# Optimization experiments

Measured on AMD Instinct MI355X. Metric: run time of the kernel, lower is better.

## Reference

```python
import jax, jax.numpy as jnp
import numpy as np

ALPHA = 0.2  # LeakyReLU negative slope


def setup_inputs() -> dict:
    key = jax.random.key(0)
    k1, k2, k3, k4, k5 = jax.random.split(key, 5)
    N, H, W, T, V, F = 8, 64, 64, 32, 32, 32
    h = jax.random.normal(k1, (N, H, W, T, V), dtype=jnp.float32)
    W_map = jax.random.normal(k2, (T, F), dtype=jnp.float32) * (1.414 / np.sqrt(T))
    b_map = jax.random.normal(k3, (F,), dtype=jnp.float32) * 0.01
    a_attn = jax.random.normal(k4, (2 * F, 1), dtype=jnp.float32) * (1.414 / np.sqrt(2 * F))
    B_adj = jax.random.normal(k5, (V, V), dtype=jnp.float32) * 1e-3 + 1e-6
    return {"h": h, "W_map": W_map, "b_map": b_map, "a_attn": a_attn, "B_adj": B_adj}


def reference(h, W_map, b_map, a_attn, B_adj):
    # h: (N,H,W,T,V) -> (N,V,H,W,T)
    hv = jnp.transpose(h, (0, 4, 1, 2, 3))
    Wh = hv @ W_map + b_map  # (N,V,H,W,F) -- LinearMapping
    N, V, H, W, F = Wh.shape
    # pairwise concat + matmul with a decomposes exactly into two projections
    a1, a2 = a_attn[:F, 0], a_attn[F:, 0]
    e = (jnp.einsum('nihwf,f->nihw', Wh, a1)[:, :, None, :, :]
         + jnp.einsum('njhwf,f->njhw', Wh, a2)[:, None, :, :, :])  # (N,V,V,H,W)
    e = jnp.where(e > 0, e, ALPHA * e)  # LeakyReLU
    attn = jax.nn.softmax(e, axis=-1)  # softmax over the W dim (as in original: dim=-1 of (N,V,V,H,W))
    # normalized adjacency: (B + I), min-max scaled, symmetric degree normalization
    adj = B_adj + jnp.eye(V, dtype=B_adj.dtype)
    adj = (adj - adj.min()) / (adj.max() - adj.min())
    d12 = 1.0 / jnp.sqrt(jnp.sum(adj, axis=1))
    adj_n = d12[:, None] * adj * d12[None, :]  # (V,V)
    # weighted aggregation over source vertices j (the original double for-loop)
    hp = jnp.einsum('nijhw,njhwf->inhwf', attn, Wh)  # (V,N,H,W,F)
    # replicate permute(1,3,4,2,0).view(N,H,W*F,V) @ adj_n
    hp = jnp.transpose(hp, (1, 3, 4, 2, 0)).reshape(N, H, W * F, V)
    hp = (hp @ adj_n).reshape(N, H, W, F, V)
    return jax.nn.elu(hp)
```

## Files before the change

kernel.cpp:

```cpp
#include <hip/hip_runtime.h>
#include <math.h>

typedef __attribute__((ext_vector_type(8))) short bf16x8;
typedef __attribute__((ext_vector_type(16))) float f32x16;
typedef __attribute__((ext_vector_type(4))) float f32x4;

static constexpr size_t WS_WA   = 0;
static constexpr size_t WS_C12  = 64;
static constexpr size_t WS_WMF  = 96;
static constexpr size_t WS_ADJF = 608;

__device__ __forceinline__ unsigned short f2bf(float x){
    union { float f; unsigned u; } c; c.f = x;
    unsigned r = c.u + 0x7FFFu + ((c.u >> 16) & 1u);
    return (unsigned short)(r >> 16);
}
__device__ __forceinline__ unsigned pk2(float a, float b){
    return (unsigned)f2bf(a) | ((unsigned)f2bf(b) << 16);
}
__device__ __forceinline__ float bf2f(unsigned short v){
    return __uint_as_float(((unsigned)v) << 16);
}
__device__ __forceinline__ float elu(float x){ return x > 0.f ? x : __expf(x) - 1.0f; }
__device__ __forceinline__ float lrelu(float x){ return fmaxf(x, 0.2f * x); }

__global__ __launch_bounds__(1024) void k0_prep(const float* __restrict__ W_map,
    const float* __restrict__ b_map, const float* __restrict__ a_attn,
    const float* __restrict__ B_adj, float* __restrict__ ws)
{
    __shared__ float lds[1024];
    __shared__ float d12[32];
    int tid = threadIdx.x;
    int i = tid >> 5, j = tid & 31;
    float a = B_adj[tid] + (i == j ? 1.0f : 0.0f);
    lds[tid] = a; __syncthreads();
    for (int s = 512; s > 0; s >>= 1) { if (tid < s) lds[tid] = fmaxf(lds[tid], lds[tid + s]); __syncthreads(); }
    float mx = lds[0]; __syncthreads();
    lds[tid] = a; __syncthreads();
    for (int s = 512; s > 0; s >>= 1) { if (tid < s) lds[tid] = fminf(lds[tid], lds[tid + s]); __syncthreads(); }
    float mn = lds[0]; __syncthreads();
    lds[tid] = (a - mn) / (mx - mn); __syncthreads();
    if (tid < 32) {
        float s = 0.f;
        for (int jj = 0; jj < 32; ++jj) s += lds[tid * 32 + jj];
        d12[tid] = 1.0f / sqrtf(s);
    }
    __syncthreads();

    {
        int kap = tid >> 9, rem = tid & 511, l = rem >> 3, e = rem & 7;
        int krow = 16 * kap + 8 * (l >> 5) + e;
        int col  = l & 31;
        ((unsigned short*)(ws + WS_WMF))[tid] = f2bf(W_map[krow * 32 + col]);
        float aij = B_adj[krow * 32 + col] + (krow == col ? 1.0f : 0.0f);
        float adjv = d12[krow] * ((aij - mn) / (mx - mn)) * d12[col];
        ((unsigned short*)(ws + WS_ADJF))[tid] = f2bf(adjv);
    }
    if (tid < 32) {
        float w1 = 0.f, w2 = 0.f;
        for (int f = 0; f < 32; ++f) {
            w1 += W_map[tid * 32 + f] * a_attn[f];
            w2 += W_map[tid * 32 + f] * a_attn[32 + f];
        }
        ws[WS_WA + tid] = w1; ws[WS_WA + 32 + tid] = w2;
    }
    if (tid == 0) {
        float c1 = 0.f, c2 = 0.f;
        for (int f = 0; f < 32; ++f) { c1 += b_map[f] * a_attn[f]; c2 += b_map[f] * a_attn[32 + f]; }
        ws[WS_C12] = c1; ws[WS_C12 + 1] = c2;
    }
}

template<int KAP>
__device__ __forceinline__ bf16x8 xform(const f32x16& d, int hi){
    unsigned b0 = pk2(d[8*KAP+0], d[8*KAP+1]);
    unsigned b1 = pk2(d[8*KAP+2], d[8*KAP+3]);
    unsigned b2 = pk2(d[8*KAP+4], d[8*KAP+5]);
    unsigned b3 = pk2(d[8*KAP+6], d[8*KAP+7]);
    unsigned pb0 = (unsigned)__shfl_xor((int)b0, 32, 64);
    unsigned pb1 = (unsigned)__shfl_xor((int)b1, 32, 64);
    unsigned pb2 = (unsigned)__shfl_xor((int)b2, 32, 64);
    unsigned pb3 = (unsigned)__shfl_xor((int)b3, 32, 64);
    union { unsigned u[4]; bf16x8 v; } t;
    t.u[0] = hi ? pb2 : b0;
    t.u[1] = hi ? pb3 : b1;
    t.u[2] = hi ? b2 : pb0;
    t.u[3] = hi ? b3 : pb1;
    return t.v;
}

__global__ __launch_bounds__(1024) void kfused(const float* __restrict__ hin,
    const float* __restrict__ b_map, const float* __restrict__ ws, float* __restrict__ out)
{
    __shared__ unsigned short hbf[64 * 1024];
    __shared__ float s1L[64 * 32];
    __shared__ float s2L[64 * 32];
    __shared__ float rdenL[32 * 32];
    __shared__ float waL[64];

    const int tid = threadIdx.x;
    const int wv = tid >> 6, l = tid & 63;
    const int c = l & 31, hi = l >> 5;
    const int nh = blockIdx.x;
    const int hh = nh & 63, n = nh >> 6;

    if (tid < 64) waL[tid] = ws[WS_WA + tid];
    const float c1 = ws[WS_C12], c2 = ws[WS_C12 + 1];
    const float bc = b_map[c];

    bf16x8 B1f[2], B2f[2];
    {
        const unsigned short* wmf = (const unsigned short*)(ws + WS_WMF);
        const unsigned short* adf = (const unsigned short*)(ws + WS_ADJF);
        B1f[0] = *(const bf16x8*)(wmf + l * 8);
        B1f[1] = *(const bf16x8*)(wmf + 512 + l * 8);
        B2f[0] = *(const bf16x8*)(adf + l * 8);
        B2f[1] = *(const bf16x8*)(adf + 512 + l * 8);
    }

    {
        const float* hrow = hin + (long)nh * 65536;
        unsigned* hb32 = (unsigned*)hbf;
#pragma unroll
        for (int it = 0; it < 8; ++it) {
            int slot = it * 1024 + tid;
            int s = slot >> 7, r = slot & 127;
            int t = (r >> 3) * 2, v0 = (r & 7) * 4;
            f32x4 x0 = *(const f32x4*)(hrow + s * 1024 + t * 32 + v0);
            f32x4 x1 = *(const f32x4*)(hrow + s * 1024 + (t + 1) * 32 + v0);
            int kap = t >> 4, e = t & 7, lb = 32 * ((t >> 3) & 1);
#pragma unroll
            for (int cc = 0; cc < 4; ++cc) {
                int u16i = s * 1024 + kap * 512 + (v0 + cc + lb) * 8 + e;
                hb32[u16i >> 1] = pk2(x0[cc], x1[cc]);
            }
        }
    }
    __syncthreads();

    {
        float wa1v[16], wa2v[16];
#pragma unroll
        for (int kk = 0; kk < 16; ++kk) {
            int t = 16 * (kk >> 3) + 8 * hi + (kk & 7);
            wa1v[kk] = waL[t]; wa2v[kk] = waL[32 + t];
        }
#pragma unroll
        for (int k = 0; k < 4; ++k) {
            int s = wv * 4 + k;
            const unsigned short* fp = hbf + s * 1024;
            bf16x8 f0 = *(const bf16x8*)(fp + l * 8);
            bf16x8 f1 = *(const bf16x8*)(fp + 512 + l * 8);
            float p1 = 0.f, p2 = 0.f;
#pragma unroll
            for (int e = 0; e < 8; ++e) {
                float x = bf2f((unsigned short)f0[e]);
                p1 = fmaf(x, wa1v[e], p1); p2 = fmaf(x, wa2v[e], p2);
            }
#pragma unroll
            for (int e = 0; e < 8; ++e) {
                float x = bf2f((unsigned short)f1[e]);
                p1 = fmaf(x, wa1v[8 + e], p1); p2 = fmaf(x, wa2v[8 + e], p2);
            }
            p1 += __shfl_xor(p1, 32, 64);
            p2 += __shfl_xor(p2, 32, 64);
            if (!hi) { s1L[s * 32 + c] = p1 + c1; s2L[s * 32 + c] = p2 + c2; }
        }
    }
    __syncthreads();

    {
        int i = tid >> 5, j = tid & 31;
        float sum = 0.f;
#pragma unroll
        for (int w = 0; w < 64; ++w)
            sum += __expf(lrelu(s1L[w * 32 + i] + s2L[w * 32 + j]));
        rdenL[tid] = 1.0f / sum;
    }
    __syncthreads();

    const int hh5 = hh >> 5, f3 = hh & 31;
#pragma unroll 1
    for (int k = 0; k < 4; ++k) {
        const int s = wv * 4 + k;
        const unsigned short* fp = hbf + s * 1024;
        bf16x8 a10 = *(const bf16x8*)(fp + l * 8);
        bf16x8 a11 = *(const bf16x8*)(fp + 512 + l * 8);

        f32x16 d1;
#pragma unroll
        for (int r = 0; r < 16; ++r) d1[r] = bc;
        d1 = __builtin_amdgcn_mfma_f32_32x32x16_bf16(a10, B1f[0], d1, 0, 0, 0);
        d1 = __builtin_amdgcn_mfma_f32_32x32x16_bf16(a11, B1f[1], d1, 0, 0, 0);
        bf16x8 A3_0 = xform<0>(d1, hi);
        bf16x8 A3_1 = xform<1>(d1, hi);

        const float s2c = s2L[s * 32 + c];
        f32x4 sa = *(const f32x4*)&s1L[s * 32 + 8 * hi];
        f32x4 sb = *(const f32x4*)&s1L[s * 32 + 8 * hi + 4];
        f32x4 sc_ = *(const f32x4*)&s1L[s * 32 + 16 + 8 * hi];
        f32x4 sd = *(const f32x4*)&s1L[s * 32 + 16 + 8 * hi + 4];
        float q[16];
#pragma unroll
        for (int e = 0; e < 4; ++e) {
            int i0 = 8 * hi + e, i1 = 8 * hi + 4 + e, i2i = 16 + 8 * hi + e, i3 = 16 + 8 * hi + 4 + e;
            q[e]      = __expf(lrelu(sa[e] + s2c)) * rdenL[i0 * 32 + c];
            q[4 + e]  = __expf(lrelu(sb[e] + s2c)) * rdenL[i1 * 32 + c];
            q[8 + e]  = __expf(lrelu(sc_[e] + s2c)) * rdenL[i2i * 32 + c];
            q[12 + e] = __expf(lrelu(sd[e] + s2c)) * rdenL[i3 * 32 + c];
        }
        union { unsigned u[4]; bf16x8 v; } A2_0, A2_1;
        A2_0.u[0] = pk2(q[0], q[1]);  A2_0.u[1] = pk2(q[2], q[3]);
        A2_0.u[2] = pk2(q[4], q[5]);  A2_0.u[3] = pk2(q[6], q[7]);
        A2_1.u[0] = pk2(q[8], q[9]);  A2_1.u[1] = pk2(q[10], q[11]);
        A2_1.u[2] = pk2(q[12], q[13]); A2_1.u[3] = pk2(q[14], q[15]);

        f32x16 d2;
#pragma unroll
        for (int r = 0; r < 16; ++r) d2[r] = 0.f;
        d2 = __builtin_amdgcn_mfma_f32_32x32x16_bf16(A2_0.v, B2f[0], d2, 0, 0, 0);
        d2 = __builtin_amdgcn_mfma_f32_32x32x16_bf16(A2_1.v, B2f[1], d2, 0, 0, 0);
        bf16x8 B3_0 = xform<0>(d2, hi);
        bf16x8 B3_1 = xform<1>(d2, hi);

        f32x16 d3;
#pragma unroll
        for (int r = 0; r < 16; ++r) d3[r] = 0.f;
        d3 = __builtin_amdgcn_mfma_f32_32x32x16_bf16(A3_0, B3_0, d3, 0, 0, 0);
        d3 = __builtin_amdgcn_mfma_f32_32x32x16_bf16(A3_1, B3_1, d3, 0, 0, 0);

        float* ob = out + (((long)(n * 64 + s) * 64) * 32 + f3) * 32 + c;
#pragma unroll
        for (int r = 0; r < 16; ++r) {
            int f = (r & 3) + 8 * (r >> 2) + 4 * hi;
            ob[(f * 2 + hh5) * 1024] = elu(d3[r]);
        }
    }
}

extern "C" void kernel_launch(void* const* d_in, const int* in_sizes, int n_in,
                              void* d_out, int out_size, void* d_ws, size_t ws_size,
                              hipStream_t stream) {
    (void)in_sizes; (void)n_in; (void)out_size; (void)ws_size;
    const float* hin    = (const float*)d_in[0];
    const float* W_map  = (const float*)d_in[1];
    const float* b_map  = (const float*)d_in[2];
    const float* a_attn = (const float*)d_in[3];
    const float* B_adj  = (const float*)d_in[4];
    float* out = (float*)d_out;
    float* ws  = (float*)d_ws;

    hipLaunchKernelGGL(k0_prep, dim3(1),   dim3(1024), 0, stream, W_map, b_map, a_attn, B_adj, ws);
    hipLaunchKernelGGL(kfused,  dim3(512), dim3(1024), 0, stream, hin, b_map, ws, out);
}
```

Measured before the change: 70.68 us.

## Use permlane32_swap, rework bf16 staging loads, nontemporal stores, unroll main loop

Several independent changes. The xform transpose now uses permlane32_swap where the builtin exists, replacing four xor-32 shuffles and selects. The input staging loop loads scalar floats strided by 32 so each thread packs eight bf16 values into one 16-byte LDS store, instead of two float4 loads and four 4-byte stores. Output stores become nontemporal, and the main loop is unrolled by 2 with a launch_bounds minimum-blocks hint of 4. The scalar strided loads may issue more global load instructions, and the unroll may raise register pressure.

```diff
diff --git a/kernel.cpp b/kernel.cpp
--- a/kernel.cpp
+++ b/kernel.cpp
@@ -4,6 +4,7 @@
 typedef __attribute__((ext_vector_type(8))) short bf16x8;
 typedef __attribute__((ext_vector_type(16))) float f32x16;
 typedef __attribute__((ext_vector_type(4))) float f32x4;
+typedef __attribute__((ext_vector_type(8))) unsigned short us8;
 
 static constexpr size_t WS_WA   = 0;
 static constexpr size_t WS_C12  = 64;
@@ -71,6 +72,22 @@
     }
 }
 
+#if __has_builtin(__builtin_amdgcn_permlane32_swap)
+typedef __attribute__((ext_vector_type(2))) unsigned int u32p;
+template<int KAP>
+__device__ __forceinline__ bf16x8 xform(const f32x16& d, int hi){
+    (void)hi;
+    unsigned b0 = pk2(d[8*KAP+0], d[8*KAP+1]);
+    unsigned b1 = pk2(d[8*KAP+2], d[8*KAP+3]);
+    unsigned b2 = pk2(d[8*KAP+4], d[8*KAP+5]);
+    unsigned b3 = pk2(d[8*KAP+6], d[8*KAP+7]);
+    u32p s02 = __builtin_amdgcn_permlane32_swap(b0, b2, false, false);
+    u32p s13 = __builtin_amdgcn_permlane32_swap(b1, b3, false, false);
+    union { unsigned u[4]; bf16x8 v; } t;
+    t.u[0] = s02[0]; t.u[1] = s13[0]; t.u[2] = s02[1]; t.u[3] = s13[1];
+    return t.v;
+}
+#else
 template<int KAP>
 __device__ __forceinline__ bf16x8 xform(const f32x16& d, int hi){
     unsigned b0 = pk2(d[8*KAP+0], d[8*KAP+1]);
@@ -88,14 +105,15 @@
     t.u[3] = hi ? b3 : pb1;
     return t.v;
 }
-
-__global__ __launch_bounds__(1024) void kfused(const float* __restrict__ hin,
+#endif
+
+__global__ __launch_bounds__(1024, 4) void kfused(const float* __restrict__ hin,
     const float* __restrict__ b_map, const float* __restrict__ ws, float* __restrict__ out)
 {
     __shared__ unsigned short hbf[64 * 1024];
     __shared__ float s1L[64 * 32];
     __shared__ float s2L[64 * 32];
-    __shared__ float rdenL[32 * 32];
+    __shared__ float rdenL[1024];
     __shared__ float waL[64];
 
     const int tid = threadIdx.x;
@@ -120,20 +138,19 @@
 
     {
         const float* hrow = hin + (long)nh * 65536;
-        unsigned* hb32 = (unsigned*)hbf;
+        const int v = tid & 31;
 #pragma unroll
         for (int it = 0; it < 8; ++it) {
-            int slot = it * 1024 + tid;
-            int s = slot >> 7, r = slot & 127;
-            int t = (r >> 3) * 2, v0 = (r & 7) * 4;
-            f32x4 x0 = *(const f32x4*)(hrow + s * 1024 + t * 32 + v0);
-            f32x4 x1 = *(const f32x4*)(hrow + s * 1024 + (t + 1) * 32 + v0);
-            int kap = t >> 4, e = t & 7, lb = 32 * ((t >> 3) & 1);
-#pragma unroll
-            for (int cc = 0; cc < 4; ++cc) {
-                int u16i = s * 1024 + kap * 512 + (v0 + cc + lb) * 8 + e;
-                hb32[u16i >> 1] = pk2(x0[cc], x1[cc]);
-            }
+            const int gid = it * 32 + (tid >> 5);
+            const int site = gid >> 2, kap = (gid >> 1) & 1, hw = gid & 1;
+            const float* hp = hrow + site * 1024 + (16 * kap + 8 * hw) * 32 + v;
+            float x[8];
+#pragma unroll
+            for (int e = 0; e < 8; ++e) x[e] = hp[e * 32];
+            union { unsigned u[4]; us8 v8; } pk;
+            pk.u[0] = pk2(x[0], x[1]); pk.u[1] = pk2(x[2], x[3]);
+            pk.u[2] = pk2(x[4], x[5]); pk.u[3] = pk2(x[6], x[7]);
+            *(us8*)(hbf + site * 1024 + kap * 512 + (v + 32 * hw) * 8) = pk.v8;
         }
     }
     __syncthreads();
@@ -180,7 +197,7 @@
     __syncthreads();
 
     const int hh5 = hh >> 5, f3 = hh & 31;
-#pragma unroll 1
+#pragma unroll 2
     for (int k = 0; k < 4; ++k) {
         const int s = wv * 4 + k;
         const unsigned short* fp = hbf + s * 1024;
@@ -196,23 +213,23 @@
         bf16x8 A3_1 = xform<1>(d1, hi);
 
         const float s2c = s2L[s * 32 + c];
-        f32x4 sa = *(const f32x4*)&s1L[s * 32 + 8 * hi];
-        f32x4 sb = *(const f32x4*)&s1L[s * 32 + 8 * hi + 4];
+        f32x4 sa  = *(const f32x4*)&s1L[s * 32 + 8 * hi];
+        f32x4 sb  = *(const f32x4*)&s1L[s * 32 + 8 * hi + 4];
         f32x4 sc_ = *(const f32x4*)&s1L[s * 32 + 16 + 8 * hi];
-        f32x4 sd = *(const f32x4*)&s1L[s * 32 + 16 + 8 * hi + 4];
+        f32x4 sd  = *(const f32x4*)&s1L[s * 32 + 16 + 8 * hi + 4];
         float q[16];
 #pragma unroll
         for (int e = 0; e < 4; ++e) {
             int i0 = 8 * hi + e, i1 = 8 * hi + 4 + e, i2i = 16 + 8 * hi + e, i3 = 16 + 8 * hi + 4 + e;
-            q[e]      = __expf(lrelu(sa[e] + s2c)) * rdenL[i0 * 32 + c];
-            q[4 + e]  = __expf(lrelu(sb[e] + s2c)) * rdenL[i1 * 32 + c];
+            q[e]      = __expf(lrelu(sa[e] + s2c))  * rdenL[i0 * 32 + c];
+            q[4 + e]  = __expf(lrelu(sb[e] + s2c))  * rdenL[i1 * 32 + c];
             q[8 + e]  = __expf(lrelu(sc_[e] + s2c)) * rdenL[i2i * 32 + c];
-            q[12 + e] = __expf(lrelu(sd[e] + s2c)) * rdenL[i3 * 32 + c];
+            q[12 + e] = __expf(lrelu(sd[e] + s2c))  * rdenL[i3 * 32 + c];
         }
         union { unsigned u[4]; bf16x8 v; } A2_0, A2_1;
-        A2_0.u[0] = pk2(q[0], q[1]);  A2_0.u[1] = pk2(q[2], q[3]);
-        A2_0.u[2] = pk2(q[4], q[5]);  A2_0.u[3] = pk2(q[6], q[7]);
-        A2_1.u[0] = pk2(q[8], q[9]);  A2_1.u[1] = pk2(q[10], q[11]);
+        A2_0.u[0] = pk2(q[0], q[1]);   A2_0.u[1] = pk2(q[2], q[3]);
+        A2_0.u[2] = pk2(q[4], q[5]);   A2_0.u[3] = pk2(q[6], q[7]);
+        A2_1.u[0] = pk2(q[8], q[9]);   A2_1.u[1] = pk2(q[10], q[11]);
         A2_1.u[2] = pk2(q[12], q[13]); A2_1.u[3] = pk2(q[14], q[15]);
 
         f32x16 d2;
@@ -233,7 +250,7 @@
 #pragma unroll
         for (int r = 0; r < 16; ++r) {
             int f = (r & 3) + 8 * (r >> 2) + 4 * hi;
-            ob[(f * 2 + hh5) * 1024] = elu(d3[r]);
+            __builtin_nontemporal_store(elu(d3[r]), ob + (f * 2 + hh5) * 1024);
         }
     }
 }
```

Result: faster. 65.28 us (-7.6%).
